# Performance work log

Hardware: AMD Instinct MI355X
Metric: run time of the kernel (lower is better)

## Reference

```python
import jax, jax.numpy as jnp
import numpy as np

N_HEAD = 12
NEG_BIG = 1e10  # additive mask constant from the source


def setup_inputs() -> dict:
    key = jax.random.key(0)
    k1, k2, k3 = jax.random.split(key, 3)
    B, S, D = 8, 1024, 768
    x = jax.random.normal(k1, (B, S, D), dtype=jnp.float32)
    W_attn = jax.random.normal(k2, (D, 3 * D), dtype=jnp.float32) * 0.02
    W_proj = jax.random.normal(k3, (D, D), dtype=jnp.float32) * 0.02
    return {"x": x, "W_attn": W_attn, "W_proj": W_proj}


def reference(x, W_attn, W_proj):
    B, S, D = x.shape
    H = N_HEAD
    dh = D // H  # head dim = 64

    c = x @ W_attn                       # [B, S, 3D]
    q, k, v = jnp.split(c, 3, axis=-1)   # each [B, S, D]

    def split_heads(t):
        return t.reshape(B, S, H, dh).transpose(0, 2, 1, 3)  # [B, H, S, dh]

    q, k, v = split_heads(q), split_heads(k), split_heads(v)

    scale = 1.0 / jnp.sqrt(jnp.asarray(dh, q.dtype))
    a = jnp.einsum('bhqd,bhkd->bhqk', q, k) * scale  # [B, H, S, S]

    # causal mask: i >= j - ns + nd with nd == ns -> lower triangular
    i = jnp.arange(S)[:, None]
    j = jnp.arange(S)[None, :]
    m = (i >= j).astype(a.dtype)  # [S, S]
    a = a * m - (1.0 - m) * NEG_BIG

    a = jax.nn.softmax(a, axis=-1)

    out = jnp.einsum('bhqk,bhkd->bhqd', a, v)        # [B, H, S, dh]
    out = out.transpose(0, 2, 1, 3).reshape(B, S, D)  # merge heads
    return out @ W_proj
```

## Files before the change

kernel.cpp:

```cpp
#include <hip/hip_runtime.h>
#include <hip/hip_bf16.h>

typedef __attribute__((ext_vector_type(4))) float f32x4;
typedef __attribute__((ext_vector_type(8))) short short8;
typedef unsigned short u16;
typedef unsigned int u32;

__device__ __forceinline__ u16 f2bf(float f) {
    u32 u = __float_as_uint(f);
    u32 r = (u + 0x7fffu + ((u >> 16) & 1u)) >> 16;
    return (u16)r;
}
__device__ __forceinline__ u32 pack2bf(float a, float b) {
    __hip_bfloat162 w = __float22bfloat162_rn(float2{a, b});
    return *(u32*)&w;
}
__device__ __forceinline__ void stage16(const u16* gsrc, u16* ldsdst) {
    __builtin_amdgcn_global_load_lds((const __attribute__((address_space(1))) void*)gsrc,
                                     (__attribute__((address_space(3))) void*)ldsdst, 16, 0, 0);
}

__global__ __launch_bounds__(256) void conv_f32_bf16(const float* __restrict__ in,
                                                     u16* __restrict__ out, int n4) {
    int i = blockIdx.x * 256 + threadIdx.x;
    int stride = gridDim.x * 256;
    for (; i < n4; i += stride) {
        float4 v = ((const float4*)in)[i];
        ushort4 o;
        o.x = f2bf(v.x); o.y = f2bf(v.y); o.z = f2bf(v.z); o.w = f2bf(v.w);
        ((ushort4*)out)[i] = o;
    }
}

__global__ __launch_bounds__(256) void conv_transpose(const float* __restrict__ W,
                                                      u16* __restrict__ Wt, int K, int N) {
    __shared__ float tile[64][65];
    int n0 = blockIdx.x * 64, k0 = blockIdx.y * 64;
    int c = threadIdx.x & 63, r0 = threadIdx.x >> 6;
#pragma unroll
    for (int i = 0; i < 16; ++i) {
        int r = r0 * 16 + i;
        tile[r][c] = W[(size_t)(k0 + r) * N + n0 + c];
    }
    __syncthreads();
#pragma unroll
    for (int i = 0; i < 16; ++i) {
        int r = r0 * 16 + i;
        Wt[(size_t)(n0 + r) * K + k0 + c] = f2bf(tile[c][r]);
    }
}

template <int MODE, int WM>
__global__ __launch_bounds__(256, 2) void gemmT(const u16* __restrict__ A,
                                                const u16* __restrict__ Bt,
                                                u16* __restrict__ q, u16* __restrict__ kk,
                                                u16* __restrict__ v, float* __restrict__ outf,
                                                int nby) {
    const int K = 768;
    const int BM = 2 * WM;
    __shared__ __align__(16) u16 As[2][BM * 32];
    __shared__ __align__(16) u16 Bs[2][128 * 32];
    int nwg = gridDim.x;
    int bid = blockIdx.x;
    int wgid = (bid & 7) * (nwg >> 3) + (bid >> 3);
    int mb = wgid / nby, nb = wgid % nby;
    int m0 = mb * BM, n0 = nb * 128;
    int tid = threadIdx.x;
    int wave = tid >> 6, lane = tid & 63;
    int lo = lane & 15, hi = lane >> 4;
    int wm = (wave >> 1) * WM, wn = (wave & 1) * 64;
    int srow = lane >> 2, scol = (lane & 3) * 8;
    f32x4 acc[WM / 16][4] = {};
    const u16* Ab = A + (size_t)(m0 + (WM / 2) * wave + srow) * K + scol;
    const u16* Bb = Bt + (size_t)(n0 + 32 * wave + srow) * K + scol;
    const int ldsAoff = ((WM / 2) * wave) * 32;
    const int ldsBoff = (32 * wave) * 32;

    auto stage = [&](int bufi, int k0) {
#pragma unroll
        for (int c = 0; c < WM / 32; ++c)
            stage16(Ab + k0 + (size_t)(16 * c) * K, &As[bufi][ldsAoff + 16 * c * 32]);
#pragma unroll
        for (int c = 0; c < 2; ++c)
            stage16(Bb + k0 + (size_t)(16 * c) * K, &Bs[bufi][ldsBoff + 16 * c * 32]);
    };
    auto compute = [&](int bufi) {
        short8 af[WM / 16], bf[4];
#pragma unroll
        for (int i = 0; i < WM / 16; ++i)
            af[i] = *(const short8*)&As[bufi][(wm + 16 * i + lo) * 32 + hi * 8];
#pragma unroll
        for (int j = 0; j < 4; ++j)
            bf[j] = *(const short8*)&Bs[bufi][(wn + 16 * j + lo) * 32 + hi * 8];
#pragma unroll
        for (int i = 0; i < WM / 16; ++i)
#pragma unroll
            for (int j = 0; j < 4; ++j)
                acc[i][j] = __builtin_amdgcn_mfma_f32_16x16x32_bf16(af[i], bf[j], acc[i][j], 0, 0, 0);
    };

    stage(0, 0);
    __syncthreads();
    int cur = 0;
    for (int k0 = 32; k0 < K; k0 += 32) {
        stage(cur ^ 1, k0);
        compute(cur);
        __syncthreads();
        cur ^= 1;
    }
    compute(cur);

    if (MODE == 0) {
        int ncb = n0 + wn;
        int which = ncb / 768;
        int h = (ncb % 768) >> 6;
        if (which == 2) {
#pragma unroll
            for (int i = 0; i < WM / 16; ++i) {
                int mrow = m0 + wm + 16 * i + 4 * hi;
                int b = mrow >> 10, s0 = mrow & 1023;
                size_t bh = (size_t)(b * 12 + h);
#pragma unroll
                for (int j = 0; j < 4; ++j) {
                    uint2 pk;
                    pk.x = pack2bf(acc[i][j][0], acc[i][j][1]);
                    pk.y = pack2bf(acc[i][j][2], acc[i][j][3]);
                    *(uint2*)&v[(bh * 64 + 16 * j + lo) * 1024 + s0] = pk;
                }
            }
        } else {
            u16* dst = (which == 0) ? q : kk;
            float scale = (which == 0) ? 0.18033688f : 1.0f;
#pragma unroll
            for (int i = 0; i < WM / 16; ++i) {
#pragma unroll
                for (int r = 0; r < 4; ++r) {
                    int mrow = m0 + wm + 16 * i + 4 * hi + r;
                    int b = mrow >> 10, s = mrow & 1023;
                    size_t bh = (size_t)(b * 12 + h);
#pragma unroll
                    for (int j = 0; j < 4; ++j)
                        dst[(bh * 1024 + s) * 64 + 16 * j + lo] = f2bf(acc[i][j][r] * scale);
                }
            }
        }
    } else {
#pragma unroll
        for (int i = 0; i < WM / 16; ++i)
#pragma unroll
            for (int j = 0; j < 4; ++j)
#pragma unroll
                for (int r = 0; r < 4; ++r) {
                    int mrow = m0 + wm + 16 * i + 4 * hi + r;
                    int ncol = n0 + wn + 16 * j + lo;
                    outf[(size_t)mrow * 768 + ncol] = acc[i][j][r];
                }
    }
}

__global__ __launch_bounds__(256) void attn_fwd(const u16* __restrict__ qg,
                                                const u16* __restrict__ kg,
                                                const u16* __restrict__ vg,
                                                u16* __restrict__ ab) {
    __shared__ __align__(16) u16 Kl[2][64 * 64];
    __shared__ __align__(16) u16 Vl[2][64 * 64];
    __shared__ __align__(16) u16 P[4][16][72];
    int tid = threadIdx.x, wave = tid >> 6, lane = tid & 63;
    int lo = lane & 15, hi = lane >> 4;
    int bid = blockIdx.x;
    int j = bid >> 3;
    int bh = (bid & 7) * 12 + (j >> 3);
    int qp = j & 7;
    int b = bh / 12, h = bh % 12;
    u16(*Pw)[72] = P[wave];
    int srow = lane >> 3;
    int schunk = (lane & 7) ^ srow;
    const u16* kA = kg + ((size_t)bh << 16) + (size_t)(16 * wave + srow) * 64 + schunk * 8;
    const u16* vA = vg + ((size_t)bh << 16) + (size_t)(16 * wave + srow) * 1024 + schunk * 8;
    int sw0 = (hi ^ (lo & 7)) * 8;
    int sw1 = ((4 + hi) ^ (lo & 7)) * 8;

    auto stageKV = [&](int bufi, int kv0) {
        u16* kD = Kl[bufi] + wave * 1024;
        u16* vD = Vl[bufi] + wave * 1024;
        stage16(kA + (size_t)kv0 * 64, kD);
        stage16(kA + (size_t)kv0 * 64 + 512, kD + 512);
        stage16(vA + kv0, vD);
        stage16(vA + kv0 + 8 * 1024, vD + 512);
    };

#pragma unroll 1
    for (int part = 0; part < 2; ++part) {
        int qblk = part ? (15 - qp) : qp;
        int q0 = qblk * 64 + 16 * wave;
        const u16* qrow = qg + ((size_t)bh * 1024 + q0 + lo) * 64 + hi * 8;
        short8 qf0 = *(const short8*)qrow;
        short8 qf1 = *(const short8*)(qrow + 32);
        f32x4 acc[4] = {};
        float lsum = 0.f;
        int nt = qblk + 1;
        stageKV(0, 0);
        __syncthreads();
        int cur = 0;
#pragma unroll 1
        for (int t = 0; t < nt; ++t) {
            int kv0 = t * 64;
            if (t + 1 < nt) stageKV(cur ^ 1, kv0 + 64);
            f32x4 st[4] = {};
#pragma unroll
            for (int f = 0; f < 4; ++f) {
                const u16* kp = &Kl[cur][(16 * f + lo) * 64];
                short8 k0 = *(const short8*)(kp + sw0);
                short8 k1 = *(const short8*)(kp + sw1);
                st[f] = __builtin_amdgcn_mfma_f32_16x16x32_bf16(k0, qf0, st[f], 0, 0, 0);
                st[f] = __builtin_amdgcn_mfma_f32_16x16x32_bf16(k1, qf1, st[f], 0, 0, 0);
            }
            if (t == nt - 1) {
#pragma unroll
                for (int f = 0; f < 4; ++f) {
                    int kvb = kv0 + 16 * f + 4 * hi;
#pragma unroll
                    for (int r = 0; r < 4; ++r)
                        if (kvb + r > q0 + lo) st[f][r] = -1e30f;
                }
            }
#pragma unroll
            for (int f = 0; f < 4; ++f) {
                float p0 = exp2f(st[f][0]);
                float p1 = exp2f(st[f][1]);
                float p2 = exp2f(st[f][2]);
                float p3 = exp2f(st[f][3]);
                lsum += (p0 + p1) + (p2 + p3);
                uint2 wv;
                wv.x = pack2bf(p0, p1);
                wv.y = pack2bf(p2, p3);
                *(uint2*)&Pw[lo][16 * f + 4 * hi] = wv;
            }
            asm volatile("s_waitcnt lgkmcnt(0)" ::: "memory");
#pragma unroll
            for (int c = 0; c < 2; ++c) {
                short8 pb = *(const short8*)&Pw[lo][c * 32 + hi * 8];
                int sw = c ? sw1 : sw0;
#pragma unroll
                for (int f2 = 0; f2 < 4; ++f2) {
                    short8 vf = *(const short8*)(&Vl[cur][(16 * f2 + lo) * 64] + sw);
                    acc[f2] = __builtin_amdgcn_mfma_f32_16x16x32_bf16(vf, pb, acc[f2], 0, 0, 0);
                }
            }
            __syncthreads();
            cur ^= 1;
        }
        lsum += __shfl_xor(lsum, 16);
        lsum += __shfl_xor(lsum, 32);
        float inv = 1.0f / lsum;
        u16* orow = ab + ((size_t)b * 1024 + q0 + lo) * 768 + h * 64 + 4 * hi;
#pragma unroll
        for (int f2 = 0; f2 < 4; ++f2) {
            uint2 wv;
            wv.x = pack2bf(acc[f2][0] * inv, acc[f2][1] * inv);
            wv.y = pack2bf(acc[f2][2] * inv, acc[f2][3] * inv);
            *(uint2*)(orow + 16 * f2) = wv;
        }
    }
}

extern "C" void kernel_launch(void* const* d_in, const int* in_sizes, int n_in,
                              void* d_out, int out_size, void* d_ws, size_t ws_size,
                              hipStream_t stream) {
    const float* x = (const float*)d_in[0];
    const float* Wa = (const float*)d_in[1];
    const float* Wp = (const float*)d_in[2];
    float* out = (float*)d_out;
    char* ws = (char*)d_ws;
    const size_t SZ = (size_t)8 * 1024 * 768 * 2;
    u16* xb = (u16*)ws;
    u16* qb = (u16*)(ws + SZ);
    u16* kb = (u16*)(ws + 2 * SZ);
    u16* vb = (u16*)(ws + 3 * SZ);
    u16* ab = (u16*)(ws + 4 * SZ);
    u16* wat = (u16*)(ws + 5 * SZ);
    u16* wpt = (u16*)(ws + 5 * SZ + (size_t)2304 * 768 * 2);

    conv_f32_bf16<<<2048, 256, 0, stream>>>(x, xb, (8 * 1024 * 768) / 4);
    conv_transpose<<<dim3(36, 12), 256, 0, stream>>>(Wa, wat, 768, 2304);
    conv_transpose<<<dim3(12, 12), 256, 0, stream>>>(Wp, wpt, 768, 768);
    gemmT<0, 128><<<576, 256, 0, stream>>>(xb, wat, qb, kb, vb, nullptr, 18);
    attn_fwd<<<768, 256, 0, stream>>>(qb, kb, vb, ab);
    gemmT<1, 64><<<384, 256, 0, stream>>>(ab, wpt, nullptr, nullptr, nullptr, out, 6);
}
```

Before: 114.8 us.

## Fuse prep kernels, shrink GEMM tiles, raise occupancy, prioritize MFMA waves

Merges the bf16 conversion of x and the two weight transposes into one launch, removing two kernel launches. Both GEMMs switch to smaller M tiles (WM 64 and 32) with twice as many workgroups and launch_bounds raised to 4 blocks per CU, trading per-block data reuse for more parallelism and occupancy. s_setprio hints are placed around the MFMA sections in the GEMM and attention kernels so waves issuing matrix ops get scheduling priority. Smaller tiles increase global and LDS traffic per FLOP, and the higher occupancy bound may force register spills.

```diff
diff --git a/kernel.cpp b/kernel.cpp
--- a/kernel.cpp
+++ b/kernel.cpp
@@ -20,38 +20,51 @@
                                      (__attribute__((address_space(3))) void*)ldsdst, 16, 0, 0);
 }
 
-__global__ __launch_bounds__(256) void conv_f32_bf16(const float* __restrict__ in,
-                                                     u16* __restrict__ out, int n4) {
-    int i = blockIdx.x * 256 + threadIdx.x;
-    int stride = gridDim.x * 256;
-    for (; i < n4; i += stride) {
-        float4 v = ((const float4*)in)[i];
-        ushort4 o;
-        o.x = f2bf(v.x); o.y = f2bf(v.y); o.z = f2bf(v.z); o.w = f2bf(v.w);
-        ((ushort4*)out)[i] = o;
+__global__ __launch_bounds__(256) void prep(const float* __restrict__ x,
+                                            const float* __restrict__ Wa,
+                                            const float* __restrict__ Wp,
+                                            u16* __restrict__ xb, u16* __restrict__ wat,
+                                            u16* __restrict__ wpt) {
+    __shared__ float tile[64][65];
+    int blk = blockIdx.x;
+    if (blk < 576) {
+        const float* W;
+        u16* Wt;
+        int N, bx, by;
+        if (blk < 432) {
+            W = Wa; Wt = wat; N = 2304; bx = blk % 36; by = blk / 36;
+        } else {
+            int i = blk - 432;
+            W = Wp; Wt = wpt; N = 768; bx = i % 12; by = i / 12;
+        }
+        int n0 = bx * 64, k0 = by * 64;
+        int c = threadIdx.x & 63, r0 = threadIdx.x >> 6;
+#pragma unroll
+        for (int i = 0; i < 16; ++i) {
+            int r = r0 * 16 + i;
+            tile[r][c] = W[(size_t)(k0 + r) * N + n0 + c];
+        }
+        __syncthreads();
+#pragma unroll
+        for (int i = 0; i < 16; ++i) {
+            int r = r0 * 16 + i;
+            Wt[(size_t)(n0 + r) * 768 + k0 + c] = f2bf(tile[c][r]);
+        }
+    } else {
+        const int n4 = (8 * 1024 * 768) / 4;
+        int i = (blk - 576) * 256 + threadIdx.x;
+        int stride = 1024 * 256;
+        for (; i < n4; i += stride) {
+            float4 v = ((const float4*)x)[i];
+            ushort4 o;
+            o.x = f2bf(v.x); o.y = f2bf(v.y); o.z = f2bf(v.z); o.w = f2bf(v.w);
+            ((ushort4*)xb)[i] = o;
+        }
     }
 }
 
-__global__ __launch_bounds__(256) void conv_transpose(const float* __restrict__ W,
-                                                      u16* __restrict__ Wt, int K, int N) {
-    __shared__ float tile[64][65];
-    int n0 = blockIdx.x * 64, k0 = blockIdx.y * 64;
-    int c = threadIdx.x & 63, r0 = threadIdx.x >> 6;
-#pragma unroll
-    for (int i = 0; i < 16; ++i) {
-        int r = r0 * 16 + i;
-        tile[r][c] = W[(size_t)(k0 + r) * N + n0 + c];
-    }
-    __syncthreads();
-#pragma unroll
-    for (int i = 0; i < 16; ++i) {
-        int r = r0 * 16 + i;
-        Wt[(size_t)(n0 + r) * K + k0 + c] = f2bf(tile[c][r]);
-    }
-}
-
 template <int MODE, int WM>
-__global__ __launch_bounds__(256, 2) void gemmT(const u16* __restrict__ A,
+__global__ __launch_bounds__(256, 4) void gemmT(const u16* __restrict__ A,
                                                 const u16* __restrict__ Bt,
                                                 u16* __restrict__ q, u16* __restrict__ kk,
                                                 u16* __restrict__ v, float* __restrict__ outf,
@@ -92,11 +105,13 @@
 #pragma unroll
         for (int j = 0; j < 4; ++j)
             bf[j] = *(const short8*)&Bs[bufi][(wn + 16 * j + lo) * 32 + hi * 8];
+        __builtin_amdgcn_s_setprio(1);
 #pragma unroll
         for (int i = 0; i < WM / 16; ++i)
 #pragma unroll
             for (int j = 0; j < 4; ++j)
                 acc[i][j] = __builtin_amdgcn_mfma_f32_16x16x32_bf16(af[i], bf[j], acc[i][j], 0, 0, 0);
+        __builtin_amdgcn_s_setprio(0);
     };
 
     stage(0, 0);
@@ -207,6 +222,7 @@
             int kv0 = t * 64;
             if (t + 1 < nt) stageKV(cur ^ 1, kv0 + 64);
             f32x4 st[4] = {};
+            __builtin_amdgcn_s_setprio(1);
 #pragma unroll
             for (int f = 0; f < 4; ++f) {
                 const u16* kp = &Kl[cur][(16 * f + lo) * 64];
@@ -215,6 +231,7 @@
                 st[f] = __builtin_amdgcn_mfma_f32_16x16x32_bf16(k0, qf0, st[f], 0, 0, 0);
                 st[f] = __builtin_amdgcn_mfma_f32_16x16x32_bf16(k1, qf1, st[f], 0, 0, 0);
             }
+            __builtin_amdgcn_s_setprio(0);
             if (t == nt - 1) {
 #pragma unroll
                 for (int f = 0; f < 4; ++f) {
@@ -237,6 +254,7 @@
                 *(uint2*)&Pw[lo][16 * f + 4 * hi] = wv;
             }
             asm volatile("s_waitcnt lgkmcnt(0)" ::: "memory");
+            __builtin_amdgcn_s_setprio(1);
 #pragma unroll
             for (int c = 0; c < 2; ++c) {
                 short8 pb = *(const short8*)&Pw[lo][c * 32 + hi * 8];
@@ -247,6 +265,7 @@
                     acc[f2] = __builtin_amdgcn_mfma_f32_16x16x32_bf16(vf, pb, acc[f2], 0, 0, 0);
                 }
             }
+            __builtin_amdgcn_s_setprio(0);
             __syncthreads();
             cur ^= 1;
         }
@@ -281,10 +300,8 @@
     u16* wat = (u16*)(ws + 5 * SZ);
     u16* wpt = (u16*)(ws + 5 * SZ + (size_t)2304 * 768 * 2);
 
-    conv_f32_bf16<<<2048, 256, 0, stream>>>(x, xb, (8 * 1024 * 768) / 4);
-    conv_transpose<<<dim3(36, 12), 256, 0, stream>>>(Wa, wat, 768, 2304);
-    conv_transpose<<<dim3(12, 12), 256, 0, stream>>>(Wp, wpt, 768, 768);
-    gemmT<0, 128><<<576, 256, 0, stream>>>(xb, wat, qb, kb, vb, nullptr, 18);
+    prep<<<1600, 256, 0, stream>>>(x, Wa, Wp, xb, wat, wpt);
+    gemmT<0, 64><<<1152, 256, 0, stream>>>(xb, wat, qb, kb, vb, nullptr, 18);
     attn_fwd<<<768, 256, 0, stream>>>(qb, kb, vb, ab);
-    gemmT<1, 64><<<384, 256, 0, stream>>>(ab, wpt, nullptr, nullptr, nullptr, out, 6);
-}
+    gemmT<1, 32><<<768, 256, 0, stream>>>(ab, wpt, nullptr, nullptr, nullptr, out, 6);
+}
```

Result: no change. 116.4 us (+1.4%).
